# Performance work log

Hardware: AMD Instinct MI355X
Metric: run time of the kernel (lower is better)

Reference implementation:

```python
import jax, jax.numpy as jnp
import numpy as np

N_NODES = 100000


def _gcn_conv(x, w, b, edge_index, n):
    # Linear transform
    x = x @ w + b
    # Add self loops
    loops = jnp.tile(jnp.arange(n, dtype=edge_index.dtype), (2, 1))
    ei = jnp.concatenate([edge_index, loops], axis=1)
    src, tgt = ei[0], ei[1]
    # Degree of source nodes (every node has a self loop -> deg >= 1)
    deg = jax.ops.segment_sum(jnp.ones(src.shape, x.dtype), src, num_segments=n)
    dinv = deg ** -0.5
    norm = dinv[src] * dinv[tgt]  # [E+N]
    # Gather-scale-scatter: out[t] += norm_e * x[s]
    msgs = norm[:, None] * x[src]  # [E+N, out_ch]
    return jax.ops.segment_sum(msgs, tgt, num_segments=n)


def setup_inputs() -> dict:
    key = jax.random.key(0)
    ks = jax.random.split(key, 6)
    n, f_in, hid, n_cls, e = N_NODES, 512, 16, 40, 3200000
    x = jax.random.normal(ks[0], (n, f_in), dtype=jnp.float32)
    edge_index = jax.random.randint(ks[1], (2, e), 0, n, dtype=jnp.int64)
    w1 = jax.random.normal(ks[2], (f_in, hid), dtype=jnp.float32) * (1.0 / np.sqrt(f_in))
    b1 = jax.random.normal(ks[3], (hid,), dtype=jnp.float32) * 0.01
    w2 = jax.random.normal(ks[4], (hid, n_cls), dtype=jnp.float32) * (1.0 / np.sqrt(hid))
    b2 = jax.random.normal(ks[5], (n_cls,), dtype=jnp.float32) * 0.01
    return {"x": x, "edge_index": edge_index, "w1": w1, "b1": b1, "w2": w2, "b2": b2}


def reference(x, edge_index, w1, b1, w2, b2):
    n = x.shape[0]
    h = _gcn_conv(x, w1, b1, edge_index, n)
    h = jax.nn.relu(h)
    # dropout is identity in eval mode (F.dropout with training=False)
    h = _gcn_conv(h, w2, b2, edge_index, n)
    return jax.nn.log_softmax(h, axis=1)
```

## Files before the change

kernel.cpp:

```cpp
#include <hip/hip_runtime.h>
#include <hip/hip_fp16.h>
#include <cstdint>

#define FIN 512
#define HID 16
#define NCLS 40
#define SHIFT 8
#define NBCAP 512
#define NBLK 512
#define BR 64
#define KC 32
#define CAP 12288
#define FCAP 12288

typedef int   iv4 __attribute__((ext_vector_type(4)));
typedef float fv4 __attribute__((ext_vector_type(4)));



__global__ void zerocur_kernel(int* __restrict__ gcur) {
    int t = threadIdx.x;
    gcur[t] = 0;
    gcur[NBCAP + t] = 0;
}


__global__ void fused_scatter_kernel(const int* __restrict__ ei, int E, int nb,
                                     int* __restrict__ gcur,
                                     unsigned char* __restrict__ tmp_src,
                                     unsigned int* __restrict__ tmp_tgt) {
    __shared__ int hs[NBCAP], ht[NBCAP];
    int t = threadIdx.x;
    for (int j = t; j < NBCAP; j += 256) { hs[j] = 0; ht[j] = 0; }
    __syncthreads();
    if ((E & 3) == 0) {
        const iv4* s4 = (const iv4*)ei;
        const iv4* t4 = (const iv4*)(ei + E);
        int E4 = E >> 2;
        int per = (E4 + NBLK - 1) / NBLK;
        int lo = blockIdx.x * per;
        int hi = lo + per; if (hi > E4) hi = E4;
        for (int i = lo + t; i < hi; i += 256) {
            iv4 s = s4[i];
            iv4 tt = t4[i];
            atomicAdd(&hs[s.x >> SHIFT], 1); atomicAdd(&hs[s.y >> SHIFT], 1);
            atomicAdd(&hs[s.z >> SHIFT], 1); atomicAdd(&hs[s.w >> SHIFT], 1);
            atomicAdd(&ht[tt.x >> SHIFT], 1); atomicAdd(&ht[tt.y >> SHIFT], 1);
            atomicAdd(&ht[tt.z >> SHIFT], 1); atomicAdd(&ht[tt.w >> SHIFT], 1);
        }
        __syncthreads();
        for (int j = t; j < nb; j += 256) {
            int v = hs[j];
            int base = atomicAdd(&gcur[j], v);
            hs[j] = j * CAP + base;
            int w = ht[j];
            int baset = atomicAdd(&gcur[NBCAP + j], w);
            ht[j] = j * CAP + baset;
        }
        __syncthreads();
        for (int i = lo + t; i < hi; i += 256) {
            iv4 s = s4[i];
            iv4 tt = t4[i];
            int p;
            p = atomicAdd(&hs[s.x >> SHIFT], 1); tmp_src[p] = (unsigned char)(s.x & 255);
            p = atomicAdd(&hs[s.y >> SHIFT], 1); tmp_src[p] = (unsigned char)(s.y & 255);
            p = atomicAdd(&hs[s.z >> SHIFT], 1); tmp_src[p] = (unsigned char)(s.z & 255);
            p = atomicAdd(&hs[s.w >> SHIFT], 1); tmp_src[p] = (unsigned char)(s.w & 255);
            p = atomicAdd(&ht[tt.x >> SHIFT], 1); tmp_tgt[p] = ((unsigned int)(tt.x & 255) << 17) | (unsigned int)s.x;
            p = atomicAdd(&ht[tt.y >> SHIFT], 1); tmp_tgt[p] = ((unsigned int)(tt.y & 255) << 17) | (unsigned int)s.y;
            p = atomicAdd(&ht[tt.z >> SHIFT], 1); tmp_tgt[p] = ((unsigned int)(tt.z & 255) << 17) | (unsigned int)s.z;
            p = atomicAdd(&ht[tt.w >> SHIFT], 1); tmp_tgt[p] = ((unsigned int)(tt.w & 255) << 17) | (unsigned int)s.w;
        }
    } else {
        int per = (E + NBLK - 1) / NBLK;
        int lo = blockIdx.x * per;
        int hi = lo + per; if (hi > E) hi = E;
        for (int i = lo + t; i < hi; i += 256) {
            atomicAdd(&hs[ei[i] >> SHIFT], 1);
            atomicAdd(&ht[ei[E + i] >> SHIFT], 1);
        }
        __syncthreads();
        for (int j = t; j < nb; j += 256) {
            int v = hs[j];
            int base = atomicAdd(&gcur[j], v);
            hs[j] = j * CAP + base;
            int w = ht[j];
            int baset = atomicAdd(&gcur[NBCAP + j], w);
            ht[j] = j * CAP + baset;
        }
        __syncthreads();
        for (int i = lo + t; i < hi; i += 256) {
            int s = ei[i], tg = ei[E + i];
            int ps = atomicAdd(&hs[s >> SHIFT], 1);
            tmp_src[ps] = (unsigned char)(s & 255);
            int pt = atomicAdd(&ht[tg >> SHIFT], 1);
            tmp_tgt[pt] = ((unsigned int)(tg & 255) << 17) | (unsigned int)s;
        }
    }
}


__global__ void bucketscan_kernel(const int* __restrict__ gcur, int nb,
                                  int* __restrict__ tgt_base,
                                  int* __restrict__ row_ptr, int N, int E) {
    __shared__ int tmp[512];
    int t = threadIdx.x;
    int v = (t < nb) ? gcur[NBCAP + t] : 0;
    tmp[t] = v;
    __syncthreads();
    for (int off = 1; off < 512; off <<= 1) {
        int a = (t >= off) ? tmp[t - off] : 0;
        __syncthreads();
        tmp[t] += a;
        __syncthreads();
    }
    if (t < nb) tgt_base[t] = tmp[t] - v;
    if (t == 0) { tgt_base[nb] = E; row_ptr[N] = E; }
}


__global__ void fine_kernel(const unsigned char* __restrict__ tmp_src,
                            const unsigned int* __restrict__ tmp_tgt,
                            const int* __restrict__ gcur,
                            const int* __restrict__ tgt_base,
                            float* __restrict__ dinv, int* __restrict__ row_ptr,
                            int* __restrict__ edges, int N) {
    __shared__ unsigned int stage[FCAP];
    __shared__ int hist[256];
    __shared__ int h2[256];
    __shared__ int scan[256];
    int b = blockIdx.x;
    int t = threadIdx.x;
    int scnt = gcur[b];
    int cnt  = gcur[NBCAP + b];
    int sb0 = b * CAP;
    int beg = tgt_base[b];
    bool staged = (cnt <= FCAP);
    hist[t] = 0;
    h2[t] = 0;
    __syncthreads();
    if (staged)
        for (int i = t; i < cnt; i += 256) stage[i] = tmp_tgt[sb0 + i];
    for (int i = t; i < scnt; i += 256)
        atomicAdd(&hist[tmp_src[sb0 + i]], 1);
    __syncthreads();
    int node = b * 256 + t;
    if (node < N) dinv[node] = rsqrtf((float)(hist[t] + 1));
    if (staged) {
        for (int i = t; i < cnt; i += 256) atomicAdd(&h2[stage[i] >> 17], 1);
    } else {
        for (int i = t; i < cnt; i += 256) atomicAdd(&h2[tmp_tgt[sb0 + i] >> 17], 1);
    }
    __syncthreads();
    int v = h2[t];
    scan[t] = v;
    __syncthreads();
    for (int off = 1; off < 256; off <<= 1) {
        int a = (t >= off) ? scan[t - off] : 0;
        __syncthreads();
        scan[t] += a;
        __syncthreads();
    }
    int ex = scan[t] - v;
    if (node < N) row_ptr[node] = beg + ex;
    h2[t] = ex;
    __syncthreads();
    if (staged) {
        for (int i = t; i < cnt; i += 256) {
            unsigned int w = stage[i];
            int tl = (int)(w >> 17);
            edges[beg + atomicAdd(&h2[tl], 1)] = (int)(w & 0x1FFFF);
        }
    } else {
        for (int i = t; i < cnt; i += 256) {
            unsigned int w = tmp_tgt[sb0 + i];
            int tl = (int)(w >> 17);
            edges[beg + atomicAdd(&h2[tl], 1)] = (int)(w & 0x1FFFF);
        }
    }
}


__global__ __launch_bounds__(256, 4)
void linear1_kernel(const float* __restrict__ x, const float* __restrict__ w1,
                    const float* __restrict__ b1, const float* __restrict__ dinv,
                    __half* __restrict__ h1h, int n) {
    __shared__ float xs[KC][BR + 2];
    __shared__ float wsc[KC * HID];
    __shared__ float bl[HID];
    int t = threadIdx.x;
    if (t < HID) bl[t] = b1[t];
    int row0 = blockIdx.x * BR;
    int rp = t >> 2;
    int cq = (t & 3) * 4;
    float acc[4] = {0, 0, 0, 0};

    fv4 xp[2];
    float wp[2];
    int rr_[2], kk_[2];
#pragma unroll
    for (int u = 0; u < 2; ++u) {
        int i = t + u * 256;
        rr_[u] = i >> 3;
        kk_[u] = (i & 7) * 4;
    }
    auto prefetch = [&](int kc) {
#pragma unroll
        for (int u = 0; u < 2; ++u) {
            int grow = row0 + rr_[u];
            if (grow < n) {
                xp[u] = __builtin_nontemporal_load((const fv4*)(x + (size_t)grow * FIN + kc + kk_[u]));
            } else {
                xp[u] = (fv4){0.f, 0.f, 0.f, 0.f};
            }
        }
        wp[0] = w1[kc * HID + t];
        wp[1] = w1[kc * HID + t + 256];
    };

    prefetch(0);
    for (int kc = 0; kc < FIN; kc += KC) {
        __syncthreads();
#pragma unroll
        for (int u = 0; u < 2; ++u) {
            xs[kk_[u] + 0][rr_[u]] = xp[u].x;
            xs[kk_[u] + 1][rr_[u]] = xp[u].y;
            xs[kk_[u] + 2][rr_[u]] = xp[u].z;
            xs[kk_[u] + 3][rr_[u]] = xp[u].w;
        }
        wsc[t] = wp[0];
        wsc[t + 256] = wp[1];
        __syncthreads();
        if (kc + KC < FIN) prefetch(kc + KC);
#pragma unroll 8
        for (int k = 0; k < KC; ++k) {
            float xv = xs[k][rp];
            float4 wv = *(const float4*)&wsc[k * HID + cq];
            acc[0] = fmaf(xv, wv.x, acc[0]);
            acc[1] = fmaf(xv, wv.y, acc[1]);
            acc[2] = fmaf(xv, wv.z, acc[2]);
            acc[3] = fmaf(xv, wv.w, acc[3]);
        }
    }
    int r0 = row0 + rp;
    if (r0 < n) {
        float dv = dinv[r0];
        __half2* hp = (__half2*)(h1h + (size_t)r0 * HID + cq);
        hp[0] = __floats2half2_rn(dv * (acc[0] + bl[cq + 0]), dv * (acc[1] + bl[cq + 1]));
        hp[1] = __floats2half2_rn(dv * (acc[2] + bl[cq + 2]), dv * (acc[3] + bl[cq + 3]));
    }
}


__global__ void agg1_kernel(const __half* __restrict__ in, const int* __restrict__ edges,
                            const int* __restrict__ row_ptr, const float* __restrict__ dinv,
                            __half* __restrict__ out16, float* __restrict__ rowsum, int n) {
    int gid = blockIdx.x * blockDim.x + threadIdx.x;
    int node = gid >> 5;
    int sub = (gid >> 3) & 3;
    int c2 = gid & 7;
    if (node >= n) return;
    const __half2* tab = (const __half2*)in;
    float dv = dinv[node];
    float a0 = 0.f, a1 = 0.f, rs = 0.f;
    if (sub == 0) {
        float2 sv = __half22float2(tab[(size_t)node * 8 + c2]);
        a0 = sv.x; a1 = sv.y; rs = dv;
    }
    int beg = row_ptr[node], end = row_ptr[node + 1];
#pragma unroll 4
    for (int i = beg + sub; i < end; i += 4) {
        int src = edges[i];
        float2 v = __half22float2(tab[(size_t)src * 8 + c2]);
        a0 += v.x;
        a1 += v.y;
        rs += dinv[src];
    }
    a0 += __shfl_xor(a0, 8);  a1 += __shfl_xor(a1, 8);  rs += __shfl_xor(rs, 8);
    a0 += __shfl_xor(a0, 16); a1 += __shfl_xor(a1, 16); rs += __shfl_xor(rs, 16);
    if (sub == 0) {
        float dv2 = dv * dv;
        a0 = fmaxf(dv2 * a0, 0.f);
        a1 = fmaxf(dv2 * a1, 0.f);
        ((__half2*)out16)[(size_t)node * 8 + c2] = __floats2half2_rn(a0, a1);
        if (c2 == 0) rowsum[node] = dv * rs;
    }
}


__global__ void agg2_kernel(const __half* __restrict__ in, const int* __restrict__ edges,
                            const int* __restrict__ row_ptr, const float* __restrict__ dinv,
                            const float* __restrict__ rowsum,
                            const float* __restrict__ w2, const float* __restrict__ b2,
                            float* __restrict__ out, int n) {
    __shared__ float g2[8][HID + 1];
    __shared__ float wl[HID * NCLS];
    __shared__ float bl[NCLS];
    int t = threadIdx.x;
    for (int i = t; i < HID * NCLS; i += 256) wl[i] = w2[i];
    if (t < NCLS) bl[t] = b2[t];
    int gid = blockIdx.x * 256 + t;
    int node = gid >> 5;
    int sub = (t >> 3) & 3;
    int c2 = t & 7;
    int nl = t >> 5;
    float a0 = 0.f, a1 = 0.f;
    float dv = 0.f;
    if (node < n) {
        const __half2* tab = (const __half2*)in;
        dv = dinv[node];
        if (sub == 0) {
            float2 sv = __half22float2(tab[(size_t)node * 8 + c2]);
            a0 = sv.x; a1 = sv.y;
        }
        int beg = row_ptr[node], end = row_ptr[node + 1];
#pragma unroll 4
        for (int i = beg + sub; i < end; i += 4) {
            int src = edges[i];
            float2 v = __half22float2(tab[(size_t)src * 8 + c2]);
            a0 += v.x;
            a1 += v.y;
        }
    }
    a0 += __shfl_xor(a0, 8);  a1 += __shfl_xor(a1, 8);
    a0 += __shfl_xor(a0, 16); a1 += __shfl_xor(a1, 16);
    if (sub == 0) { g2[nl][c2 * 2] = dv * a0; g2[nl][c2 * 2 + 1] = dv * a1; }
    __syncthreads();
    if (t < 16) {
        int nl2 = t >> 1, half = t & 1;
        int node2 = blockIdx.x * 8 + nl2;
        float z[20];
        float m = -1e30f, se = 0.f;
        if (node2 < n) {
            float h[HID];
#pragma unroll
            for (int j = 0; j < HID; ++j) h[j] = g2[nl2][j];
            float rs = rowsum[node2];
            int c0 = half * 20;
#pragma unroll
            for (int c = 0; c < 20; ++c) {
                float s = rs * bl[c0 + c];
#pragma unroll
                for (int j = 0; j < HID; ++j) s = fmaf(h[j], wl[j * NCLS + c0 + c], s);
                z[c] = s;
            }
            m = z[0];
#pragma unroll
            for (int c = 1; c < 20; ++c) m = fmaxf(m, z[c]);
        }
        m = fmaxf(m, __shfl_xor(m, 1));
        if (node2 < n) {
#pragma unroll
            for (int c = 0; c < 20; ++c) se += __expf(z[c] - m);
        }
        se += __shfl_xor(se, 1);
        if (node2 < n) {
            float lse = m + __logf(se);
            float* orow = out + (size_t)node2 * NCLS + half * 20;
#pragma unroll
            for (int c = 0; c < 20; ++c) orow[c] = z[c] - lse;
        }
    }
}


extern "C" void kernel_launch(void* const* d_in, const int* in_sizes, int n_in,
                              void* d_out, int out_size, void* d_ws, size_t ws_size,
                              hipStream_t stream) {
    const float* x  = (const float*)d_in[0];
    const int*   ei = (const int*)d_in[1];
    const float* w1 = (const float*)d_in[2];
    const float* b1 = (const float*)d_in[3];
    const float* w2 = (const float*)d_in[4];
    const float* b2 = (const float*)d_in[5];
    float* out = (float*)d_out;

    int N = in_sizes[0] / FIN;
    int E = in_sizes[1] / 2;
    int nb = (N + 255) >> SHIFT;

    char* p = (char*)d_ws;
    auto alloc = [&](size_t bytes) -> char* {
        char* r = p;
        p += (bytes + 255) / 256 * 256;
        return r;
    };
    int*   gcur      = (int*)alloc((size_t)2 * NBCAP * 4);
    int*   tgt_base  = (int*)alloc((size_t)(nb + 1) * 4);
    float* dinv      = (float*)alloc((size_t)N * 4);
    int*   row_ptr   = (int*)alloc((size_t)(N + 1) * 4);
    unsigned char* tmp_src = (unsigned char*)alloc((size_t)nb * CAP);
    unsigned int*  tmp_tgt = (unsigned int*)alloc((size_t)nb * CAP * 4);
    int*    edges    = (int*)alloc((size_t)E * 4);
    __half* h1h      = (__half*)alloc((size_t)N * HID * 2);
    __half* gh       = (__half*)alloc((size_t)N * HID * 2);
    float*  rowsum   = (float*)alloc((size_t)N * 4);

    zerocur_kernel<<<1, NBCAP, 0, stream>>>(gcur);
    fused_scatter_kernel<<<NBLK, 256, 0, stream>>>(ei, E, nb, gcur, tmp_src, tmp_tgt);
    bucketscan_kernel<<<1, 512, 0, stream>>>(gcur, nb, tgt_base, row_ptr, N, E);
    fine_kernel<<<nb, 256, 0, stream>>>(tmp_src, tmp_tgt, gcur, tgt_base,
                                        dinv, row_ptr, edges, N);
    linear1_kernel<<<(N + BR - 1) / BR, 256, 0, stream>>>(x, w1, b1, dinv, h1h, N);
    agg1_kernel<<<(N * 32 + 255) / 256, 256, 0, stream>>>(h1h, edges, row_ptr, dinv,
                                                          gh, rowsum, N);
    agg2_kernel<<<(N * 32 + 255) / 256, 256, 0, stream>>>(gh, edges, row_ptr, dinv,
                                                          rowsum, w2, b2, out, N);
}
```

Baseline: 483.8 us.

## Fold bucket scan into fine kernel and use nontemporal loads/stores for streams

Removes the single-block bucketscan kernel launch. Each fine_kernel block now computes its own bucket base offset by reducing the preceding bucket counts from gcur, and the last block writes row_ptr[N]. Streaming scratch buffers (tmp_src, tmp_tgt, edges, and the output rows) are also switched to nontemporal loads and stores to reduce cache pollution. This trades one launch and a serial dependency for redundant per-block prefix work, with some risk that nontemporal hints hurt the reuse of edges in the second aggregation pass.

```diff
diff --git a/kernel.cpp b/kernel.cpp
--- a/kernel.cpp
+++ b/kernel.cpp
@@ -62,14 +62,14 @@
             iv4 s = s4[i];
             iv4 tt = t4[i];
             int p;
-            p = atomicAdd(&hs[s.x >> SHIFT], 1); tmp_src[p] = (unsigned char)(s.x & 255);
-            p = atomicAdd(&hs[s.y >> SHIFT], 1); tmp_src[p] = (unsigned char)(s.y & 255);
-            p = atomicAdd(&hs[s.z >> SHIFT], 1); tmp_src[p] = (unsigned char)(s.z & 255);
-            p = atomicAdd(&hs[s.w >> SHIFT], 1); tmp_src[p] = (unsigned char)(s.w & 255);
-            p = atomicAdd(&ht[tt.x >> SHIFT], 1); tmp_tgt[p] = ((unsigned int)(tt.x & 255) << 17) | (unsigned int)s.x;
-            p = atomicAdd(&ht[tt.y >> SHIFT], 1); tmp_tgt[p] = ((unsigned int)(tt.y & 255) << 17) | (unsigned int)s.y;
-            p = atomicAdd(&ht[tt.z >> SHIFT], 1); tmp_tgt[p] = ((unsigned int)(tt.z & 255) << 17) | (unsigned int)s.z;
-            p = atomicAdd(&ht[tt.w >> SHIFT], 1); tmp_tgt[p] = ((unsigned int)(tt.w & 255) << 17) | (unsigned int)s.w;
+            p = atomicAdd(&hs[s.x >> SHIFT], 1); __builtin_nontemporal_store((unsigned char)(s.x & 255), &tmp_src[p]);
+            p = atomicAdd(&hs[s.y >> SHIFT], 1); __builtin_nontemporal_store((unsigned char)(s.y & 255), &tmp_src[p]);
+            p = atomicAdd(&hs[s.z >> SHIFT], 1); __builtin_nontemporal_store((unsigned char)(s.z & 255), &tmp_src[p]);
+            p = atomicAdd(&hs[s.w >> SHIFT], 1); __builtin_nontemporal_store((unsigned char)(s.w & 255), &tmp_src[p]);
+            p = atomicAdd(&ht[tt.x >> SHIFT], 1); __builtin_nontemporal_store(((unsigned int)(tt.x & 255) << 17) | (unsigned int)s.x, &tmp_tgt[p]);
+            p = atomicAdd(&ht[tt.y >> SHIFT], 1); __builtin_nontemporal_store(((unsigned int)(tt.y & 255) << 17) | (unsigned int)s.y, &tmp_tgt[p]);
+            p = atomicAdd(&ht[tt.z >> SHIFT], 1); __builtin_nontemporal_store(((unsigned int)(tt.z & 255) << 17) | (unsigned int)s.z, &tmp_tgt[p]);
+            p = atomicAdd(&ht[tt.w >> SHIFT], 1); __builtin_nontemporal_store(((unsigned int)(tt.w & 255) << 17) | (unsigned int)s.w, &tmp_tgt[p]);
         }
     } else {
         int per = (E + NBLK - 1) / NBLK;
@@ -92,39 +92,19 @@
         for (int i = lo + t; i < hi; i += 256) {
             int s = ei[i], tg = ei[E + i];
             int ps = atomicAdd(&hs[s >> SHIFT], 1);
-            tmp_src[ps] = (unsigned char)(s & 255);
+            __builtin_nontemporal_store((unsigned char)(s & 255), &tmp_src[ps]);
             int pt = atomicAdd(&ht[tg >> SHIFT], 1);
-            tmp_tgt[pt] = ((unsigned int)(tg & 255) << 17) | (unsigned int)s;
-        }
-    }
-}
-
-
-__global__ void bucketscan_kernel(const int* __restrict__ gcur, int nb,
-                                  int* __restrict__ tgt_base,
-                                  int* __restrict__ row_ptr, int N, int E) {
-    __shared__ int tmp[512];
-    int t = threadIdx.x;
-    int v = (t < nb) ? gcur[NBCAP + t] : 0;
-    tmp[t] = v;
-    __syncthreads();
-    for (int off = 1; off < 512; off <<= 1) {
-        int a = (t >= off) ? tmp[t - off] : 0;
-        __syncthreads();
-        tmp[t] += a;
-        __syncthreads();
-    }
-    if (t < nb) tgt_base[t] = tmp[t] - v;
-    if (t == 0) { tgt_base[nb] = E; row_ptr[N] = E; }
+            __builtin_nontemporal_store(((unsigned int)(tg & 255) << 17) | (unsigned int)s, &tmp_tgt[pt]);
+        }
+    }
 }
 
 
 __global__ void fine_kernel(const unsigned char* __restrict__ tmp_src,
                             const unsigned int* __restrict__ tmp_tgt,
                             const int* __restrict__ gcur,
-                            const int* __restrict__ tgt_base,
                             float* __restrict__ dinv, int* __restrict__ row_ptr,
-                            int* __restrict__ edges, int N) {
+                            int* __restrict__ edges, int N, int E, int nb) {
     __shared__ unsigned int stage[FCAP];
     __shared__ int hist[256];
     __shared__ int h2[256];
@@ -134,22 +114,31 @@
     int scnt = gcur[b];
     int cnt  = gcur[NBCAP + b];
     int sb0 = b * CAP;
-    int beg = tgt_base[b];
+    int part = 0;
+    for (int j = t; j < b; j += 256) part += gcur[NBCAP + j];
+    scan[t] = part;
+    __syncthreads();
+    for (int off = 128; off > 0; off >>= 1) {
+        if (t < off) scan[t] += scan[t + off];
+        __syncthreads();
+    }
+    int beg = scan[0];
+    __syncthreads();
     bool staged = (cnt <= FCAP);
     hist[t] = 0;
     h2[t] = 0;
     __syncthreads();
     if (staged)
-        for (int i = t; i < cnt; i += 256) stage[i] = tmp_tgt[sb0 + i];
+        for (int i = t; i < cnt; i += 256) stage[i] = __builtin_nontemporal_load(&tmp_tgt[sb0 + i]);
     for (int i = t; i < scnt; i += 256)
-        atomicAdd(&hist[tmp_src[sb0 + i]], 1);
+        atomicAdd(&hist[__builtin_nontemporal_load(&tmp_src[sb0 + i])], 1);
     __syncthreads();
     int node = b * 256 + t;
     if (node < N) dinv[node] = rsqrtf((float)(hist[t] + 1));
     if (staged) {
         for (int i = t; i < cnt; i += 256) atomicAdd(&h2[stage[i] >> 17], 1);
     } else {
-        for (int i = t; i < cnt; i += 256) atomicAdd(&h2[tmp_tgt[sb0 + i] >> 17], 1);
+        for (int i = t; i < cnt; i += 256) atomicAdd(&h2[__builtin_nontemporal_load(&tmp_tgt[sb0 + i]) >> 17], 1);
     }
     __syncthreads();
     int v = h2[t];
@@ -163,19 +152,20 @@
     }
     int ex = scan[t] - v;
     if (node < N) row_ptr[node] = beg + ex;
+    if (b == nb - 1 && t == 0) row_ptr[N] = E;
     h2[t] = ex;
     __syncthreads();
     if (staged) {
         for (int i = t; i < cnt; i += 256) {
             unsigned int w = stage[i];
             int tl = (int)(w >> 17);
-            edges[beg + atomicAdd(&h2[tl], 1)] = (int)(w & 0x1FFFF);
+            __builtin_nontemporal_store((int)(w & 0x1FFFF), &edges[beg + atomicAdd(&h2[tl], 1)]);
         }
     } else {
         for (int i = t; i < cnt; i += 256) {
-            unsigned int w = tmp_tgt[sb0 + i];
+            unsigned int w = __builtin_nontemporal_load(&tmp_tgt[sb0 + i]);
             int tl = (int)(w >> 17);
-            edges[beg + atomicAdd(&h2[tl], 1)] = (int)(w & 0x1FFFF);
+            __builtin_nontemporal_store((int)(w & 0x1FFFF), &edges[beg + atomicAdd(&h2[tl], 1)]);
         }
     }
 }
@@ -270,7 +260,7 @@
     int beg = row_ptr[node], end = row_ptr[node + 1];
 #pragma unroll 4
     for (int i = beg + sub; i < end; i += 4) {
-        int src = edges[i];
+        int src = __builtin_nontemporal_load(&edges[i]);
         float2 v = __half22float2(tab[(size_t)src * 8 + c2]);
         a0 += v.x;
         a1 += v.y;
@@ -316,7 +306,7 @@
         int beg = row_ptr[node], end = row_ptr[node + 1];
 #pragma unroll 4
         for (int i = beg + sub; i < end; i += 4) {
-            int src = edges[i];
+            int src = __builtin_nontemporal_load(&edges[i]);
             float2 v = __half22float2(tab[(size_t)src * 8 + c2]);
             a0 += v.x;
             a1 += v.y;
@@ -358,7 +348,7 @@
             float lse = m + __logf(se);
             float* orow = out + (size_t)node2 * NCLS + half * 20;
 #pragma unroll
-            for (int c = 0; c < 20; ++c) orow[c] = z[c] - lse;
+            for (int c = 0; c < 20; ++c) __builtin_nontemporal_store(z[c] - lse, &orow[c]);
         }
     }
 }
@@ -386,7 +376,6 @@
         return r;
     };
     int*   gcur      = (int*)alloc((size_t)2 * NBCAP * 4);
-    int*   tgt_base  = (int*)alloc((size_t)(nb + 1) * 4);
     float* dinv      = (float*)alloc((size_t)N * 4);
     int*   row_ptr   = (int*)alloc((size_t)(N + 1) * 4);
     unsigned char* tmp_src = (unsigned char*)alloc((size_t)nb * CAP);
@@ -398,9 +387,8 @@
 
     zerocur_kernel<<<1, NBCAP, 0, stream>>>(gcur);
     fused_scatter_kernel<<<NBLK, 256, 0, stream>>>(ei, E, nb, gcur, tmp_src, tmp_tgt);
-    bucketscan_kernel<<<1, 512, 0, stream>>>(gcur, nb, tgt_base, row_ptr, N, E);
-    fine_kernel<<<nb, 256, 0, stream>>>(tmp_src, tmp_tgt, gcur, tgt_base,
-                                        dinv, row_ptr, edges, N);
+    fine_kernel<<<nb, 256, 0, stream>>>(tmp_src, tmp_tgt, gcur,
+                                        dinv, row_ptr, edges, N, E, nb);
     linear1_kernel<<<(N + BR - 1) / BR, 256, 0, stream>>>(x, w1, b1, dinv, h1h, N);
     agg1_kernel<<<(N * 32 + 255) / 256, 256, 0, stream>>>(h1h, edges, row_ptr, dinv,
                                                           gh, rowsum, N);
```

New measurement: 745.8 us. 1.54x slower.
